# Performance work log

Hardware: AMD Instinct MI355X
Metric: run time of the kernel (lower is better)

The kernel has to match this reference:

```python
import jax, jax.numpy as jnp
import numpy as np

B, T, D, H = 64, 512, 1024, 1024

def setup_inputs() -> dict:
    key = jax.random.key(0)
    k1, k2, k3 = jax.random.split(key, 3)
    x = jax.random.normal(k1, (B, T, D), dtype=jnp.float32)
    # original uses 'uniform' initializer; small-scale weights keep sigmoid unsaturated
    kernel = jax.random.uniform(k2, (D, H), dtype=jnp.float32, minval=-0.05, maxval=0.05)
    recurrent_kernel = jax.random.uniform(k3, (H, H), dtype=jnp.float32, minval=-0.05, maxval=0.05)
    return {"x": x, "kernel": kernel, "recurrent_kernel": recurrent_kernel}

def reference(x, kernel, recurrent_kernel):
    # Precompute input projection for all timesteps in one big GEMM: [B,T,H]
    xh = jnp.einsum('btd,dh->bth', x, kernel)
    h0 = jnp.zeros((x.shape[0], recurrent_kernel.shape[0]), dtype=x.dtype)

    def step(h_prev, xh_t):
        h = jax.nn.sigmoid(xh_t + h_prev @ recurrent_kernel)
        return h, h

    # scan over time: xh transposed to [T,B,H]
    _, states = jax.lax.scan(step, h0, jnp.swapaxes(xh, 0, 1))
    return jnp.swapaxes(states, 0, 1)  # [B,T,H]
```

## Files before the change

kernel.cpp:

```cpp
#include <hip/hip_runtime.h>
#include <stdint.h>


using short8 = __attribute__((ext_vector_type(8))) short;
using bf16x8 = __attribute__((ext_vector_type(8))) __bf16;
using f32x4  = __attribute__((ext_vector_type(4))) float;

typedef unsigned short     u16;
typedef unsigned int       u32;
typedef unsigned long long u64;

#define T_  512
#define H_  1024
#define RG_ARR 8

__device__ __forceinline__ u16 f2bf(float f) {
    union { float f; u32 i; } v; v.f = f;
    u32 b = v.i + 0x7fffu + ((v.i >> 16) & 1u);
    return (u16)(b >> 16);
}
__device__ __forceinline__ f32x4 mfma_bf16_16x16x32(short8 a, short8 b, f32x4 c) {
    return __builtin_amdgcn_mfma_f32_16x16x32_bf16(
        __builtin_bit_cast(bf16x8, a), __builtin_bit_cast(bf16x8, b), c, 0, 0, 0);
}
__device__ __forceinline__ float sigmoidf(float z) {
    z = fminf(fmaxf(z, -30.f), 30.f);
    return 1.f / (1.f + __expf(-z));
}
__device__ __forceinline__ short8 cvt8(f32x4 a0, f32x4 a1) {
    short8 r;
    #pragma unroll
    for (int j = 0; j < 4; ++j) { r[j] = (short)f2bf(a0[j]); r[4 + j] = (short)f2bf(a1[j]); }
    return r;
}

__global__ __launch_bounds__(256) void gemm_xh(const float* __restrict__ X,
                                               const float* __restrict__ Kw,
                                               float* __restrict__ Y)
{
    __shared__ alignas(16) u16 Bt[64][40];
    const int tid  = threadIdx.x;
    const int lane = tid & 63;
    const int wv   = tid >> 6;
    const int quad = lane >> 4;
    const int l16  = lane & 15;
    const int m0   = blockIdx.x * 64;
    const int n0   = blockIdx.y * 64;
    const int cB   = tid & 63;
    const int kg   = tid >> 6;

    f32x4 acc[4] = {};

    for (int k0 = 0; k0 < H_; k0 += 32) {
        __syncthreads();
        short8 sv;
        #pragma unroll
        for (int jj = 0; jj < 8; ++jj)
            sv[jj] = (short)f2bf(Kw[(k0 + kg * 8 + jj) * H_ + n0 + cB]);
        *(short8*)&Bt[cB][kg * 8] = sv;
        __syncthreads();

        const f32x4* p = (const f32x4*)&X[(m0 + wv * 16 + l16) * H_ + k0 + quad * 8];
        short8 av = cvt8(p[0], p[1]);
        #pragma unroll
        for (int nt = 0; nt < 4; ++nt) {
            short8 bv = *(const short8*)&Bt[nt * 16 + l16][quad * 8];
            acc[nt] = mfma_bf16_16x16x32(av, bv, acc[nt]);
        }
    }
    #pragma unroll
    for (int nt = 0; nt < 4; ++nt)
        #pragma unroll
        for (int r = 0; r < 4; ++r)
            Y[(m0 + wv * 16 + quad * 4 + r) * H_ + n0 + nt * 16 + l16] = acc[nt][r];
}

__global__ __launch_bounds__(256) void swz(const float* __restrict__ Kr,
                                           u16* __restrict__ Wsw,
                                           u32* __restrict__ cnt)
{
    const int t    = blockIdx.x * 256 + threadIdx.x;
    if (cnt && t < 4) cnt[t * 64] = 0;
    const int lane = t & 63;
    const int kt   = (t >> 6) & 31;
    const int wv   = (t >> 11) & 1;
    const int gj   = t >> 12;
    const int quad = lane >> 4;
    const int l16  = lane & 15;
    const int col  = gj * 32 + wv * 16 + l16;
    short8 sv;
    #pragma unroll
    for (int jj = 0; jj < 8; ++jj)
        sv[jj] = (short)f2bf(Kr[(kt * 32 + quad * 8 + jj) * H_ + col]);
    *(short8*)&Wsw[t * 8] = sv;
}

__global__ __launch_bounds__(512) void scan_k(float* __restrict__ Y,
                                              const u16* __restrict__ Wsw,
                                              u16* __restrict__ hb,
                                              u32* __restrict__ cnt)
{
    const int tid  = threadIdx.x;
    const int lane = tid & 63;
    const int wv   = tid >> 6;
    const int quad = lane >> 4;
    const int l16  = lane & 15;
    const int rg   = blockIdx.x >> 3;
    const int cg   = blockIdx.x & 7;
    const int c16  = cg * 8 + wv;

    short8 wf[32];
    #pragma unroll
    for (int j2 = 0; j2 < 32; ++j2)
        wf[j2] = *(const short8*)&Wsw[(((unsigned)c16 * 32 + (unsigned)j2) * 64 + (unsigned)lane) * 8];

    u32* const bar = cnt + rg * 64;

    u16* const hbF0 = hb + rg * 16384;
    u16* const hbF1 = hb + 65536 + rg * 16384;

    const int C0    = cg * 128 + wv * 16 + quad * 4;
    const int j2w   = C0 >> 5;
    const int quadp = (C0 >> 3) & 3;
    const int half  = (C0 >> 2) & 1;
    const int wOff  = j2w * 512 + (quadp * 16 + l16) * 8 + half * 4;

    const size_t rowBase = ((size_t)(rg * 16 + l16) * T_) * H_ + (size_t)C0;

    f32x4 xh = *(const f32x4*)&Y[rowBase];

    for (int s = 0; s < T_; ++s) {
        f32x4 a0 = {}, a1 = {}, a2 = {}, a3 = {};
        if (s > 0) {
            const u16* hp = ((s - 1) & 1) ? hbF1 : hbF0;
            const u16* ap = hp + lane * 8;
            #pragma unroll
            for (int j2 = 0; j2 < 32; ++j2) {
                short8 av = *(const short8*)(ap + j2 * 512);
                switch (j2 & 3) {
                    case 0: a0 = mfma_bf16_16x16x32(wf[j2], av, a0); break;
                    case 1: a1 = mfma_bf16_16x16x32(wf[j2], av, a1); break;
                    case 2: a2 = mfma_bf16_16x16x32(wf[j2], av, a2); break;
                    default:a3 = mfma_bf16_16x16x32(wf[j2], av, a3); break;
                }
            }
        }

        f32x4 hv;
        #pragma unroll
        for (int r = 0; r < 4; ++r)
            hv[r] = sigmoidf((a0[r] + a1[r]) + (a2[r] + a3[r]) + xh[r]);

        const u64 pk = (u64)f2bf(hv[0]) | ((u64)f2bf(hv[1]) << 16)
                     | ((u64)f2bf(hv[2]) << 32) | ((u64)f2bf(hv[3]) << 48);
        u16* const hc = (s & 1) ? hbF1 : hbF0;
        __hip_atomic_store((u64*)(hc + wOff), pk, __ATOMIC_RELAXED, __HIP_MEMORY_SCOPE_AGENT);

        if (s + 1 < T_) {
            asm volatile("s_waitcnt vmcnt(0)" ::: "memory");
            __syncthreads();
            if (tid == 0)
                __hip_atomic_fetch_add(bar, 1u, __ATOMIC_RELAXED, __HIP_MEMORY_SCOPE_AGENT);
            *(f32x4*)&Y[rowBase + (size_t)s * H_] = hv;
            xh = *(const f32x4*)&Y[rowBase + (size_t)(s + 1) * H_];
            if (tid == 0) {
                const u32 tgt = (u32)(s + 1) * (u32)RG_ARR;
                while (__hip_atomic_load(bar, __ATOMIC_RELAXED, __HIP_MEMORY_SCOPE_AGENT) < tgt)
                    __builtin_amdgcn_s_sleep(1);
                if (__hip_atomic_load(bar, __ATOMIC_ACQUIRE, __HIP_MEMORY_SCOPE_AGENT) < tgt)
                    __builtin_amdgcn_s_sleep(1);
            }
            __syncthreads();
        } else {
            *(f32x4*)&Y[rowBase + (size_t)s * H_] = hv;
        }
    }
}

template<bool SW>
__global__ __launch_bounds__(128) void step_k(float* __restrict__ Y,
                                              const void* __restrict__ Wsrc,
                                              int s)
{
    const int tid  = threadIdx.x;
    const int lane = tid & 63;
    const int wv   = tid >> 6;
    const int quad = lane >> 4;
    const int l16  = lane & 15;
    const int gi   = blockIdx.x >> 5;
    const int gj   = blockIdx.x & 31;
    const int colBase = gj * 32 + wv * 16;

    f32x4 acc = {};
    if (s > 0) {
        const int abase = ((gi * 16 + l16) * T_ + (s - 1)) * H_;
        #pragma unroll 4
        for (int j2 = 0; j2 < 32; ++j2) {
            const f32x4* ap = (const f32x4*)&Y[abase + j2 * 32 + quad * 8];
            short8 av = cvt8(ap[0], ap[1]);
            short8 bv;
            if (SW) {
                bv = *(const short8*)&((const u16*)Wsrc)[(((gj * 2 + wv) * 32 + j2) * 64 + lane) * 8];
            } else {
                const float* Krf = (const float*)Wsrc;
                #pragma unroll
                for (int jj = 0; jj < 8; ++jj)
                    bv[jj] = (short)f2bf(Krf[(j2 * 32 + quad * 8 + jj) * H_ + colBase + l16]);
            }
            acc = mfma_bf16_16x16x32(av, bv, acc);
        }
    }
    #pragma unroll
    for (int r = 0; r < 4; ++r) {
        const int idx = ((gi * 16 + quad * 4 + r) * T_ + s) * H_ + colBase + l16;
        float z = acc[r] + Y[idx];
        Y[idx] = sigmoidf(z);
    }
}

extern "C" void kernel_launch(void* const* d_in, const int* in_sizes, int n_in,
                              void* d_out, int out_size, void* d_ws, size_t ws_size,
                              hipStream_t stream) {
    const float* X  = (const float*)d_in[0];
    const float* Kw = (const float*)d_in[1];
    const float* Kr = (const float*)d_in[2];
    float* Y        = (float*)d_out;

    gemm_xh<<<dim3(512, 16), dim3(256), 0, stream>>>(X, Kw, Y);

    const size_t WSW_B  = (size_t)2 * 1024 * 1024;
    const size_t HB_B   = (size_t)2 * 64 * H_ * sizeof(u16);
    const size_t needed = WSW_B + HB_B + 1024;

    if (ws_size >= needed) {
        u16* Wsw = (u16*)d_ws;
        u16* hbd = (u16*)((char*)d_ws + WSW_B);
        u32* cnt = (u32*)((char*)d_ws + WSW_B + HB_B);
        swz<<<dim3(512), dim3(256), 0, stream>>>(Kr, Wsw, cnt);
        scan_k<<<dim3(32), dim3(512), 0, stream>>>(Y, Wsw, hbd, cnt);
    } else if (ws_size >= WSW_B) {
        u16* Wsw = (u16*)d_ws;
        swz<<<dim3(512), dim3(256), 0, stream>>>(Kr, Wsw, (u32*)nullptr);
        for (int s = 0; s < T_; ++s)
            step_k<true><<<dim3(128), dim3(128), 0, stream>>>(Y, (const void*)Wsw, s);
    } else {
        for (int s = 0; s < T_; ++s)
            step_k<false><<<dim3(128), dim3(128), 0, stream>>>(Y, (const void*)Kr, s);
    }
}
```

Baseline: 3.110 ms.

## Replace block barrier and counter with per-wave flags polled by every wave

The per-step cross-block barrier changes from a shared atomic counter with __syncthreads to per-wave flag words. Each wave writes its own step number into a flag, then all 64 lanes poll the row group's 64 flags and leave the loop once every flag has reached the target. Hidden-state loads become relaxed agent-scope atomic loads so the values written by other blocks are seen. This removes two block-wide barriers and the serialized fetch_add per step, at the cost of more polling traffic and weaker ordering guarantees than the acquire load used before.

```diff
diff --git a/kernel.cpp b/kernel.cpp
--- a/kernel.cpp
+++ b/kernel.cpp
@@ -9,10 +9,10 @@
 typedef unsigned short     u16;
 typedef unsigned int       u32;
 typedef unsigned long long u64;
+using u64x2 = __attribute__((ext_vector_type(2))) u64;
 
 #define T_  512
 #define H_  1024
-#define RG_ARR 8
 
 __device__ __forceinline__ u16 f2bf(float f) {
     union { float f; u32 i; } v; v.f = f;
@@ -77,10 +77,10 @@
 
 __global__ __launch_bounds__(256) void swz(const float* __restrict__ Kr,
                                            u16* __restrict__ Wsw,
-                                           u32* __restrict__ cnt)
+                                           u32* __restrict__ fl)
 {
     const int t    = blockIdx.x * 256 + threadIdx.x;
-    if (cnt && t < 4) cnt[t * 64] = 0;
+    if (fl && t < 256) fl[t] = 0;
     const int lane = t & 63;
     const int kt   = (t >> 6) & 31;
     const int wv   = (t >> 11) & 1;
@@ -98,7 +98,7 @@
 __global__ __launch_bounds__(512) void scan_k(float* __restrict__ Y,
                                               const u16* __restrict__ Wsw,
                                               u16* __restrict__ hb,
-                                              u32* __restrict__ cnt)
+                                              u32* __restrict__ fl)
 {
     const int tid  = threadIdx.x;
     const int lane = tid & 63;
@@ -114,10 +114,11 @@
     for (int j2 = 0; j2 < 32; ++j2)
         wf[j2] = *(const short8*)&Wsw[(((unsigned)c16 * 32 + (unsigned)j2) * 64 + (unsigned)lane) * 8];
 
-    u32* const bar = cnt + rg * 64;
-
     u16* const hbF0 = hb + rg * 16384;
     u16* const hbF1 = hb + 65536 + rg * 16384;
+
+    u32* const flrg  = fl + rg * 64;
+    u32* const flMine = flrg + c16;
 
     const int C0    = cg * 128 + wv * 16 + quad * 4;
     const int j2w   = C0 >> 5;
@@ -133,10 +134,13 @@
         f32x4 a0 = {}, a1 = {}, a2 = {}, a3 = {};
         if (s > 0) {
             const u16* hp = ((s - 1) & 1) ? hbF1 : hbF0;
-            const u16* ap = hp + lane * 8;
+            const u64* ap = (const u64*)hp + (size_t)lane * 2;
             #pragma unroll
             for (int j2 = 0; j2 < 32; ++j2) {
-                short8 av = *(const short8*)(ap + j2 * 512);
+                u64x2 q;
+                q[0] = __hip_atomic_load(ap + j2 * 128 + 0, __ATOMIC_RELAXED, __HIP_MEMORY_SCOPE_AGENT);
+                q[1] = __hip_atomic_load(ap + j2 * 128 + 1, __ATOMIC_RELAXED, __HIP_MEMORY_SCOPE_AGENT);
+                short8 av = __builtin_bit_cast(short8, q);
                 switch (j2 & 3) {
                     case 0: a0 = mfma_bf16_16x16x32(wf[j2], av, a0); break;
                     case 1: a1 = mfma_bf16_16x16x32(wf[j2], av, a1); break;
@@ -158,19 +162,16 @@
 
         if (s + 1 < T_) {
             asm volatile("s_waitcnt vmcnt(0)" ::: "memory");
-            __syncthreads();
-            if (tid == 0)
-                __hip_atomic_fetch_add(bar, 1u, __ATOMIC_RELAXED, __HIP_MEMORY_SCOPE_AGENT);
+            if (lane == 0)
+                __hip_atomic_store(flMine, (u32)(s + 1), __ATOMIC_RELAXED, __HIP_MEMORY_SCOPE_AGENT);
             *(f32x4*)&Y[rowBase + (size_t)s * H_] = hv;
             xh = *(const f32x4*)&Y[rowBase + (size_t)(s + 1) * H_];
-            if (tid == 0) {
-                const u32 tgt = (u32)(s + 1) * (u32)RG_ARR;
-                while (__hip_atomic_load(bar, __ATOMIC_RELAXED, __HIP_MEMORY_SCOPE_AGENT) < tgt)
-                    __builtin_amdgcn_s_sleep(1);
-                if (__hip_atomic_load(bar, __ATOMIC_ACQUIRE, __HIP_MEMORY_SCOPE_AGENT) < tgt)
-                    __builtin_amdgcn_s_sleep(1);
+            const u32 tgt = (u32)(s + 1);
+            for (;;) {
+                u32 f = __hip_atomic_load(&flrg[lane], __ATOMIC_RELAXED, __HIP_MEMORY_SCOPE_AGENT);
+                if (__all(f >= tgt)) break;
+                __builtin_amdgcn_s_sleep(1);
             }
-            __syncthreads();
         } else {
             *(f32x4*)&Y[rowBase + (size_t)s * H_] = hv;
         }
@@ -235,9 +236,9 @@
     if (ws_size >= needed) {
         u16* Wsw = (u16*)d_ws;
         u16* hbd = (u16*)((char*)d_ws + WSW_B);
-        u32* cnt = (u32*)((char*)d_ws + WSW_B + HB_B);
-        swz<<<dim3(512), dim3(256), 0, stream>>>(Kr, Wsw, cnt);
-        scan_k<<<dim3(32), dim3(512), 0, stream>>>(Y, Wsw, hbd, cnt);
+        u32* fl  = (u32*)((char*)d_ws + WSW_B + HB_B);
+        swz<<<dim3(512), dim3(256), 0, stream>>>(Kr, Wsw, fl);
+        scan_k<<<dim3(32), dim3(512), 0, stream>>>(Y, Wsw, hbd, fl);
     } else if (ws_size >= WSW_B) {
         u16* Wsw = (u16*)d_ws;
         swz<<<dim3(512), dim3(256), 0, stream>>>(Kr, Wsw, (u32*)nullptr);
```

Result: slower. 5.282 ms (+69.8%).
